# Performance work log

Measured on AMD Instinct MI355X. Metric: run time of the kernel, lower is better.

Reference implementation:

```python
import jax, jax.numpy as jnp
import numpy as np

SUP_NUM = 2048
EPS_NORM = 1e-12
EPS_BN = 1e-5


def l2norm(v, axis):
    n = jnp.sqrt(jnp.sum(v * v, axis=axis, keepdims=True))
    return v / jnp.maximum(n, EPS_NORM)


def segment_mean(vals, ids, num_segments):
    # vals: [N, C], ids: [N] int -> [num_segments, C]
    s = jax.ops.segment_sum(vals, ids, num_segments=num_segments)
    cnt = jax.ops.segment_sum(jnp.ones((vals.shape[0],), vals.dtype), ids, num_segments=num_segments)
    return s / jnp.maximum(cnt, 1.0)[:, None]


def setup_inputs() -> dict:
    key = jax.random.key(0)
    ks = jax.random.split(key, 6)
    B, Cin, H, W = 1, 3, 1024, 1024
    Cf = 32
    x = jax.random.normal(ks[0], (B, Cin, H, W), dtype=jnp.float32)
    conv_feat = jax.random.normal(ks[1], (B, Cf, H, W), dtype=jnp.float32)
    vit_feature = jax.random.normal(ks[2], (B, SUP_NUM, Cf), dtype=jnp.float32)
    seg_ids = jax.random.randint(ks[3], (B * H * W,), 0, SUP_NUM, dtype=jnp.int32)
    w_soft = jax.random.normal(ks[4], (1, 2 * Cf, 3), dtype=jnp.float32) * 0.1
    b_soft = jnp.zeros((1,), jnp.float32)
    bn_gamma = jnp.ones((1,), jnp.float32)
    bn_beta = jnp.zeros((1,), jnp.float32)
    return {"x": x, "conv_feat": conv_feat, "vit_feature": vit_feature, "seg_ids": seg_ids,
            "w_soft": w_soft, "b_soft": b_soft, "bn_gamma": bn_gamma, "bn_beta": bn_beta}


def reference(x, conv_feat, vit_feature, seg_ids, w_soft, b_soft, bn_gamma, bn_beta):
    B, Cf, H, W = conv_feat.shape
    Cin = x.shape[1]
    # F.normalize(conv, p=2, dim=1)
    conv_1 = l2norm(conv_feat, axis=1)
    # [B,C,H,W] -> [B*H*W, C]
    F1 = conv_1.transpose(0, 2, 3, 1).reshape(-1, Cf)
    X = jax.lax.stop_gradient(x).transpose(0, 2, 3, 1).reshape(-1, Cin)
    # superpixel scatter-mean (replaces the per-segment Python loop)
    M_F = segment_mean(F1, seg_ids, SUP_NUM)                  # [Sup, Cf]
    X_F = segment_mean(X, seg_ids, SUP_NUM)                   # [Sup, Cin]
    M_F = M_F.reshape(B, SUP_NUM, Cf)
    X_F = X_F.reshape(B, SUP_NUM, Cin).transpose(0, 2, 1)     # [B, Cin, Sup]
    vit_n = l2norm(vit_feature, axis=-1)
    all_F = jnp.concatenate([M_F, vit_n], axis=-1).transpose(0, 2, 1)  # [B, 2Cf, Sup]
    all_F = l2norm(all_F, axis=1)
    # Conv1d(2Cf -> 1, k=3, pad=1)
    z = jax.lax.conv_general_dilated(all_F, w_soft, window_strides=(1,), padding=((1, 1),),
                                     dimension_numbers=("NCH", "OIH", "NCH")) + b_soft[None, :, None]
    # BatchNorm1d (training-mode batch stats over (B, L))
    mu = jnp.mean(z, axis=(0, 2), keepdims=True)
    var = jnp.mean((z - mu) ** 2, axis=(0, 2), keepdims=True)
    z = bn_gamma[None, :, None] * (z - mu) / jnp.sqrt(var + EPS_BN) + bn_beta[None, :, None]
    result = jax.nn.sigmoid(z)                                # [B, 1, Sup]
    gap = jnp.mean(result, axis=-1, keepdims=True)            # AdaptiveAvgPool1d(1)
    return (result, gap, all_F, X_F)
```

## Files before the change

### kernel.cpp

```cpp
#include <hip/hip_runtime.h>
#include <hip/hip_bf16.h>
#include <hip/hip_fp16.h>

#define SUP 2048
#define NB  256

#define SC_CONV 1024.0f
#define SC_X0   512.0f
#define SC_XLO  256.0f
#define ISC_CONV (1.0f/1024.0f)
#define ISC_X0   (1.0f/512.0f)
#define ISC_XLO  (1.0f/256.0f)

__device__ __forceinline__ int enc2i(int qa, int qb) {
    return ((qa - (qb < 0 ? 1 : 0)) << 16) + (qb & 0xFFFF);
}
__device__ __forceinline__ int enc2f(float a, float b) {
    return enc2i(__float2int_rn(a), __float2int_rn(b));
}

__global__ __launch_bounds__(1024) void k_segfused(const float* __restrict__ conv,
                                                   const float* __restrict__ x,
                                                   const int* __restrict__ ids,
                                                   float* __restrict__ accum,
                                                   __half* __restrict__ pbuf,
                                                   int npix) {
    __shared__ int sacc[18 * SUP];
    for (int i = threadIdx.x; i < 18 * SUP; i += blockDim.x) sacc[i] = 0;
    __syncthreads();

    int per = ((npix + (int)gridDim.x - 1) / (int)gridDim.x + 1) & ~1;
    int start = blockIdx.x * per;
    int end = min(start + per, npix);
    int stride2 = (int)blockDim.x * 2;

    int p = start + (int)threadIdx.x * 2;
    for (; p + 1 < end; p += stride2) {
        int2 id2 = *(const int2*)(ids + p);
        float2 cv[32];
        float s0 = 0.f, s1 = 0.f;
#pragma unroll
        for (int c = 0; c < 32; ++c) {
            cv[c] = *(const float2*)(conv + (size_t)c * npix + p);
            s0 += cv[c].x * cv[c].x;
            s1 += cv[c].y * cv[c].y;
        }
        float i0 = 1.0f / fmaxf(sqrtf(s0), 1e-12f);
        float i1 = 1.0f / fmaxf(sqrtf(s1), 1e-12f);
#pragma unroll
        for (int r = 0; r < 16; ++r) {
            float2 a = cv[2 * r], b = cv[2 * r + 1];
            atomicAdd(&sacc[r * SUP + id2.x],
                      enc2f(a.x * i0 * SC_CONV, b.x * i0 * SC_CONV));
            atomicAdd(&sacc[r * SUP + id2.y],
                      enc2f(a.y * i1 * SC_CONV, b.y * i1 * SC_CONV));
        }
        float2 x0 = *(const float2*)(x + p);
        float2 x1 = *(const float2*)(x + (size_t)npix + p);
        float2 x2 = *(const float2*)(x + (size_t)2 * npix + p);
        atomicAdd(&sacc[16 * SUP + id2.x], enc2f(x0.x * SC_X0, x1.x * SC_XLO));
        atomicAdd(&sacc[16 * SUP + id2.y], enc2f(x0.y * SC_X0, x1.y * SC_XLO));
        atomicAdd(&sacc[17 * SUP + id2.x], enc2i(1, __float2int_rn(x2.x * SC_XLO)));
        atomicAdd(&sacc[17 * SUP + id2.y], enc2i(1, __float2int_rn(x2.y * SC_XLO)));
    }
    if (p == end - 1) {
        int s = ids[p];
        float cvv[32];
        float ss = 0.f;
#pragma unroll
        for (int c = 0; c < 32; ++c) {
            cvv[c] = conv[(size_t)c * npix + p];
            ss += cvv[c] * cvv[c];
        }
        float iv = 1.0f / fmaxf(sqrtf(ss), 1e-12f);
#pragma unroll
        for (int r = 0; r < 16; ++r)
            atomicAdd(&sacc[r * SUP + s],
                      enc2f(cvv[2 * r] * iv * SC_CONV, cvv[2 * r + 1] * iv * SC_CONV));
        atomicAdd(&sacc[16 * SUP + s],
                  enc2f(x[p] * SC_X0, x[(size_t)npix + p] * SC_XLO));
        atomicAdd(&sacc[17 * SUP + s],
                  enc2i(1, __float2int_rn(x[(size_t)2 * npix + p] * SC_XLO)));
    }
    __syncthreads();

    for (int i = threadIdx.x; i < 18 * SUP; i += blockDim.x) {
        int S = sacc[i];
        int qb = (int)(short)(S & 0xFFFF);
        int qa = (S - qb) >> 16;
        int row = i >> 11;
        int s = i & (SUP - 1);
        int hi_row, lo_row;
        float fhi, flo;
        if (row < 16) {
            hi_row = 2 * row; lo_row = 2 * row + 1;
            fhi = (float)qa * ISC_CONV;
            flo = (float)qb * ISC_CONV;
        } else if (row == 16) {
            hi_row = 32; lo_row = 33;
            fhi = (float)qa * ISC_X0;
            flo = (float)qb * ISC_XLO;
        } else {
            hi_row = 35; lo_row = 34;
            fhi = (float)qa;
            flo = (float)qb * ISC_XLO;
        }
        if (pbuf) {
            __half* dst = pbuf + (size_t)blockIdx.x * 36 * SUP;
            dst[hi_row * SUP + s] = __float2half(fhi);
            dst[lo_row * SUP + s] = __float2half(flo);
        } else {
            unsafeAtomicAdd(&accum[hi_row * SUP + s], fhi);
            unsafeAtomicAdd(&accum[lo_row * SUP + s], flo);
        }
    }
}

__global__ __launch_bounds__(256) void k_reduce(const __half* __restrict__ pbuf,
                                                float* __restrict__ accum) {
    int j8 = (blockIdx.x * blockDim.x + threadIdx.x) * 8;
    if (j8 >= 36 * SUP) return;
    float s[8];
#pragma unroll
    for (int k = 0; k < 8; ++k) s[k] = 0.f;
    for (int b = 0; b < NB; ++b) {
        uint4 u = *(const uint4*)(pbuf + (size_t)b * 36 * SUP + j8);
        __half2 h0 = *reinterpret_cast<__half2*>(&u.x);
        __half2 h1 = *reinterpret_cast<__half2*>(&u.y);
        __half2 h2 = *reinterpret_cast<__half2*>(&u.z);
        __half2 h3 = *reinterpret_cast<__half2*>(&u.w);
        float2 f0 = __half22float2(h0), f1 = __half22float2(h1);
        float2 f2 = __half22float2(h2), f3 = __half22float2(h3);
        s[0] += f0.x; s[1] += f0.y; s[2] += f1.x; s[3] += f1.y;
        s[4] += f2.x; s[5] += f2.y; s[6] += f3.x; s[7] += f3.y;
    }
    float4 o0 = {s[0], s[1], s[2], s[3]};
    float4 o1 = {s[4], s[5], s[6], s[7]};
    *(float4*)(accum + j8) = o0;
    *(float4*)(accum + j8 + 4) = o1;
}

__device__ __forceinline__ void compute_col(const float* __restrict__ accum,
                                            const float* __restrict__ vit,
                                            int g, float* __restrict__ col) {
    if (g < 0 || g >= SUP) {
#pragma unroll
        for (int c = 0; c < 64; ++c) col[c] = 0.f;
        return;
    }
    float cnt = fmaxf(accum[35 * SUP + g], 1.0f);
    float rc = 1.0f / cnt;
#pragma unroll
    for (int c = 0; c < 32; ++c) col[c] = accum[c * SUP + g] * rc;
    float vs = 0.f;
#pragma unroll
    for (int c = 0; c < 32; ++c) {
        float v = vit[g * 32 + c];
        col[32 + c] = v;
        vs += v * v;
    }
    float vinv = 1.0f / fmaxf(sqrtf(vs), 1e-12f);
#pragma unroll
    for (int c = 0; c < 32; ++c) col[32 + c] *= vinv;
    float ssq = 0.f;
#pragma unroll
    for (int c = 0; c < 64; ++c) ssq += col[c] * col[c];
    float ainv = 1.0f / fmaxf(sqrtf(ssq), 1e-12f);
#pragma unroll
    for (int c = 0; c < 64; ++c) col[c] *= ainv;
}

__global__ __launch_bounds__(256) void k_finalconv(const float* __restrict__ accum,
                                                   const float* __restrict__ vit,
                                                   const float* __restrict__ w,
                                                   const float* __restrict__ bias,
                                                   float* __restrict__ allF_out,
                                                   float* __restrict__ xf_out,
                                                   float* __restrict__ z_out) {
    __shared__ float L[258][65];
    __shared__ float sw[192];
    int t = threadIdx.x;
    int b0 = blockIdx.x * 256;
    if (t < 192) sw[t] = w[t];

    float col[64];
    int g = b0 + t;
    compute_col(accum, vit, g, col);
#pragma unroll
    for (int c = 0; c < 64; ++c) L[t + 1][c] = col[c];
#pragma unroll
    for (int c = 0; c < 64; ++c) allF_out[c * SUP + g] = col[c];
    {
        float cnt = fmaxf(accum[35 * SUP + g], 1.0f);
        float rc = 1.0f / cnt;
#pragma unroll
        for (int c = 0; c < 3; ++c)
            xf_out[c * SUP + g] = accum[(32 + c) * SUP + g] * rc;
    }
    if (t == 0) {
        compute_col(accum, vit, b0 - 1, col);
#pragma unroll
        for (int c = 0; c < 64; ++c) L[0][c] = col[c];
    }
    if (t == 255) {
        compute_col(accum, vit, b0 + 256, col);
#pragma unroll
        for (int c = 0; c < 64; ++c) L[257][c] = col[c];
    }
    __syncthreads();

    float acc = bias[0];
#pragma unroll
    for (int c = 0; c < 64; ++c) {
        acc += sw[c * 3] * L[t][c] + sw[c * 3 + 1] * L[t + 1][c]
             + sw[c * 3 + 2] * L[t + 2][c];
    }
    z_out[b0 + t] = acc;
}

__global__ __launch_bounds__(512) void k_head2(const float* __restrict__ z,
                                               const float* __restrict__ gamma,
                                               const float* __restrict__ beta,
                                               float* __restrict__ out) {
    __shared__ float red[8];
    __shared__ float bc[2];
    int tid = threadIdx.x;
    int lane = tid & 63, wid = tid >> 6;

    float zs[4];
#pragma unroll
    for (int j = 0; j < 4; ++j) zs[j] = z[j * 512 + tid];

    float s1 = zs[0] + zs[1] + zs[2] + zs[3];
#pragma unroll
    for (int o = 32; o > 0; o >>= 1) s1 += __shfl_down(s1, o);
    if (lane == 0) red[wid] = s1;
    __syncthreads();
    if (tid == 0) {
        float t = 0.f;
        for (int i = 0; i < 8; ++i) t += red[i];
        bc[0] = t / (float)SUP;
    }
    __syncthreads();
    float mu = bc[0];

    float s2 = 0.f;
#pragma unroll
    for (int j = 0; j < 4; ++j) { float d = zs[j] - mu; s2 += d * d; }
#pragma unroll
    for (int o = 32; o > 0; o >>= 1) s2 += __shfl_down(s2, o);
    __syncthreads();
    if (lane == 0) red[wid] = s2;
    __syncthreads();
    if (tid == 0) {
        float t = 0.f;
        for (int i = 0; i < 8; ++i) t += red[i];
        bc[1] = t / (float)SUP;
    }
    __syncthreads();
    float var = bc[1];

    float invstd = rsqrtf(var + 1e-5f);
    float gm = gamma[0], bt = beta[0];
    float gsum = 0.f;
#pragma unroll
    for (int j = 0; j < 4; ++j) {
        int p = j * 512 + tid;
        float zn = gm * (zs[j] - mu) * invstd + bt;
        float r = 1.0f / (1.0f + expf(-zn));
        out[p] = r;
        gsum += r;
    }
#pragma unroll
    for (int o = 32; o > 0; o >>= 1) gsum += __shfl_down(gsum, o);
    __syncthreads();
    if (lane == 0) red[wid] = gsum;
    __syncthreads();
    if (tid == 0) {
        float t = 0.f;
        for (int i = 0; i < 8; ++i) t += red[i];
        out[SUP] = t / (float)SUP;
    }
}

extern "C" void kernel_launch(void* const* d_in, const int* in_sizes, int n_in,
                              void* d_out, int out_size, void* d_ws, size_t ws_size,
                              hipStream_t stream) {
    const float* x     = (const float*)d_in[0];
    const float* conv  = (const float*)d_in[1];
    const float* vit   = (const float*)d_in[2];
    const int*   ids   = (const int*)d_in[3];
    const float* w     = (const float*)d_in[4];
    const float* b     = (const float*)d_in[5];
    const float* gamma = (const float*)d_in[6];
    const float* beta  = (const float*)d_in[7];
    float* out = (float*)d_out;

    int npix = in_sizes[3];

    float* accum = (float*)d_ws;
    float* zbuf = accum + 36 * SUP;
    __half* pbuf = (__half*)(zbuf + SUP);

    size_t need = (36 * SUP + SUP) * sizeof(float)
                + (size_t)NB * 36 * SUP * sizeof(__half);
    bool useP = ws_size >= need;

    if (!useP) hipMemsetAsync(accum, 0, 36 * SUP * sizeof(float), stream);

    k_segfused<<<NB, 1024, 0, stream>>>(conv, x, ids, accum,
                                        useP ? pbuf : (__half*)nullptr, npix);
    if (useP) {
        k_reduce<<<(36 * SUP / 8 + 255) / 256, 256, 0, stream>>>(pbuf, accum);
    }

    float* allF = out + SUP + 1;
    float* xf = allF + 64 * SUP;
    k_finalconv<<<SUP / 256, 256, 0, stream>>>(accum, vit, w, b, allF, xf, zbuf);

    k_head2<<<1, 512, 0, stream>>>(zbuf, gamma, beta, out);
}
```

Measured before the change: 76.48 us.

## Split segment accumulation channels across two block groups to halve LDS usage

```diff
diff --git a/kernel.cpp b/kernel.cpp
--- a/kernel.cpp
+++ b/kernel.cpp
@@ -25,66 +25,49 @@
                                                    float* __restrict__ accum,
                                                    __half* __restrict__ pbuf,
                                                    int npix) {
-    __shared__ int sacc[18 * SUP];
-    for (int i = threadIdx.x; i < 18 * SUP; i += blockDim.x) sacc[i] = 0;
-    __syncthreads();
-
-    int per = ((npix + (int)gridDim.x - 1) / (int)gridDim.x + 1) & ~1;
+    __shared__ int sacc[9 * SUP];
+    int g = blockIdx.y;
+    for (int i = threadIdx.x; i < 9 * SUP; i += blockDim.x) sacc[i] = 0;
+    __syncthreads();
+
+    int per = (npix + (int)gridDim.x - 1) / (int)gridDim.x;
     int start = blockIdx.x * per;
     int end = min(start + per, npix);
-    int stride2 = (int)blockDim.x * 2;
-
-    int p = start + (int)threadIdx.x * 2;
-    for (; p + 1 < end; p += stride2) {
-        int2 id2 = *(const int2*)(ids + p);
-        float2 cv[32];
-        float s0 = 0.f, s1 = 0.f;
+
+    for (int p = start + (int)threadIdx.x; p < end; p += (int)blockDim.x) {
+        int s = ids[p];
+        float cv[32];
+        float ss = 0.f;
 #pragma unroll
         for (int c = 0; c < 32; ++c) {
-            cv[c] = *(const float2*)(conv + (size_t)c * npix + p);
-            s0 += cv[c].x * cv[c].x;
-            s1 += cv[c].y * cv[c].y;
-        }
-        float i0 = 1.0f / fmaxf(sqrtf(s0), 1e-12f);
-        float i1 = 1.0f / fmaxf(sqrtf(s1), 1e-12f);
-#pragma unroll
-        for (int r = 0; r < 16; ++r) {
-            float2 a = cv[2 * r], b = cv[2 * r + 1];
-            atomicAdd(&sacc[r * SUP + id2.x],
-                      enc2f(a.x * i0 * SC_CONV, b.x * i0 * SC_CONV));
-            atomicAdd(&sacc[r * SUP + id2.y],
-                      enc2f(a.y * i1 * SC_CONV, b.y * i1 * SC_CONV));
-        }
-        float2 x0 = *(const float2*)(x + p);
-        float2 x1 = *(const float2*)(x + (size_t)npix + p);
-        float2 x2 = *(const float2*)(x + (size_t)2 * npix + p);
-        atomicAdd(&sacc[16 * SUP + id2.x], enc2f(x0.x * SC_X0, x1.x * SC_XLO));
-        atomicAdd(&sacc[16 * SUP + id2.y], enc2f(x0.y * SC_X0, x1.y * SC_XLO));
-        atomicAdd(&sacc[17 * SUP + id2.x], enc2i(1, __float2int_rn(x2.x * SC_XLO)));
-        atomicAdd(&sacc[17 * SUP + id2.y], enc2i(1, __float2int_rn(x2.y * SC_XLO)));
-    }
-    if (p == end - 1) {
-        int s = ids[p];
-        float cvv[32];
-        float ss = 0.f;
-#pragma unroll
-        for (int c = 0; c < 32; ++c) {
-            cvv[c] = conv[(size_t)c * npix + p];
-            ss += cvv[c] * cvv[c];
+            cv[c] = conv[(size_t)c * npix + p];
+            ss += cv[c] * cv[c];
         }
         float iv = 1.0f / fmaxf(sqrtf(ss), 1e-12f);
-#pragma unroll
-        for (int r = 0; r < 16; ++r)
-            atomicAdd(&sacc[r * SUP + s],
-                      enc2f(cvv[2 * r] * iv * SC_CONV, cvv[2 * r + 1] * iv * SC_CONV));
-        atomicAdd(&sacc[16 * SUP + s],
-                  enc2f(x[p] * SC_X0, x[(size_t)npix + p] * SC_XLO));
-        atomicAdd(&sacc[17 * SUP + s],
-                  enc2i(1, __float2int_rn(x[(size_t)2 * npix + p] * SC_XLO)));
-    }
-    __syncthreads();
-
-    for (int i = threadIdx.x; i < 18 * SUP; i += blockDim.x) {
+        float sc = iv * SC_CONV;
+        if (g == 0) {
+#pragma unroll
+            for (int r = 0; r < 8; ++r) {
+                atomicAdd(&sacc[r * SUP + s],
+                          enc2f(cv[2 * r] * sc, cv[2 * r + 1] * sc));
+            }
+            float x0 = x[p];
+            float x1 = x[(size_t)npix + p];
+            atomicAdd(&sacc[8 * SUP + s], enc2f(x0 * SC_X0, x1 * SC_XLO));
+        } else {
+#pragma unroll
+            for (int r = 0; r < 8; ++r) {
+                atomicAdd(&sacc[r * SUP + s],
+                          enc2f(cv[16 + 2 * r] * sc, cv[17 + 2 * r] * sc));
+            }
+            float x2 = x[(size_t)2 * npix + p];
+            atomicAdd(&sacc[8 * SUP + s], enc2i(1, __float2int_rn(x2 * SC_XLO)));
+        }
+    }
+    __syncthreads();
+
+    int cb = g * 16;
+    for (int i = threadIdx.x; i < 9 * SUP; i += blockDim.x) {
         int S = sacc[i];
         int qb = (int)(short)(S & 0xFFFF);
         int qa = (S - qb) >> 16;
@@ -92,11 +75,11 @@
         int s = i & (SUP - 1);
         int hi_row, lo_row;
         float fhi, flo;
-        if (row < 16) {
-            hi_row = 2 * row; lo_row = 2 * row + 1;
+        if (row < 8) {
+            hi_row = cb + 2 * row; lo_row = hi_row + 1;
             fhi = (float)qa * ISC_CONV;
             flo = (float)qb * ISC_CONV;
-        } else if (row == 16) {
+        } else if (g == 0) {
             hi_row = 32; lo_row = 33;
             fhi = (float)qa * ISC_X0;
             flo = (float)qb * ISC_XLO;
@@ -308,7 +291,8 @@
 
     if (!useP) hipMemsetAsync(accum, 0, 36 * SUP * sizeof(float), stream);
 
-    k_segfused<<<NB, 1024, 0, stream>>>(conv, x, ids, accum,
+    dim3 g2(NB, 2);
+    k_segfused<<<g2, 1024, 0, stream>>>(conv, x, ids, accum,
                                         useP ? pbuf : (__half*)nullptr, npix);
     if (useP) {
         k_reduce<<<(36 * SUP / 8 + 255) / 256, 256, 0, stream>>>(pbuf, accum);
```

Measured after the change: 92.43 us. 1.21x slower.
